# Optimization experiments

Measured on AMD Instinct MI355X. Metric: run time of the kernel, lower is better.

The kernel has to match this reference:

```python
import jax, jax.numpy as jnp
import numpy as np

BATCH = 16384
NUM_Q = 100000
NUM_TAGS = 1024
DIFF_FEAT = 3
DIM = 64
HIDDEN = 128


def setup_inputs() -> dict:
    key = jax.random.key(0)
    ks = jax.random.split(key, 10)
    questions = jax.random.randint(ks[0], (BATCH,), 0, NUM_Q, dtype=jnp.int64 if jax.config.jax_enable_x64 else jnp.int32)
    question_skill_targets = jax.random.randint(ks[1], (BATCH, NUM_TAGS), 0, 2, dtype=jnp.int32)
    difficulty_feats = jax.random.normal(ks[2], (BATCH, DIFF_FEAT), dtype=jnp.float32)
    Q_emb = jax.random.normal(ks[3], (NUM_Q, DIM), dtype=jnp.float32) * 0.02
    S_emb = jax.random.normal(ks[4], (NUM_TAGS, DIM), dtype=jnp.float32) * 0.02
    W_diff = jax.random.normal(ks[5], (DIFF_FEAT, DIM), dtype=jnp.float32) * 0.1
    b_diff = jnp.zeros((DIM,), dtype=jnp.float32)
    W_fc = jax.random.normal(ks[6], (3 * DIM + 3, HIDDEN), dtype=jnp.float32) * 0.05
    b_fc = jnp.zeros((HIDDEN,), dtype=jnp.float32)
    W_out = jax.random.normal(ks[7], (HIDDEN, 1), dtype=jnp.float32) * 0.05
    b_out = jnp.zeros((1,), dtype=jnp.float32)
    return {"questions": questions, "question_skill_targets": question_skill_targets,
            "difficulty_feats": difficulty_feats, "Q_emb": Q_emb, "S_emb": S_emb,
            "W_diff": W_diff, "b_diff": b_diff, "W_fc": W_fc, "b_fc": b_fc,
            "W_out": W_out, "b_out": b_out}


def reference(questions, question_skill_targets, difficulty_feats,
              Q_emb, S_emb, W_diff, b_diff, W_fc, b_fc, W_out, b_out):
    # Ragged segment-mean over skill sets: mean of skill embeddings whose
    # multi-hot entry is nonzero == (T @ S) / count per row.
    t = question_skill_targets.astype(jnp.float32)            # [B, T]
    counts = jnp.sum(t, axis=1, keepdims=True)                # [B, 1] (>=1 w.h.p.)
    mu_skill = (t @ S_emb) / counts                           # [B, D]
    q = Q_emb[questions]                                      # [B, D]
    a = difficulty_feats @ W_diff + b_diff                    # [B, D]
    # PNN product layer: pairwise inner products + concat linear signals
    p12 = jnp.sum(q * mu_skill, axis=-1, keepdims=True)
    p13 = jnp.sum(q * a, axis=-1, keepdims=True)
    p23 = jnp.sum(mu_skill * a, axis=-1, keepdims=True)
    z = jnp.concatenate([q, mu_skill, a, p12, p13, p23], axis=-1)  # [B, 3D+3]
    e = jax.nn.relu(z @ W_fc + b_fc)                          # [B, H]
    p = jax.nn.sigmoid(e @ W_out + b_out)[:, 0]               # [B]
    return (e, p)
```

## Files before the change

### kernel.cpp

```cpp
#include <hip/hip_runtime.h>
#include <hip/hip_bf16.h>

#define BATCH   16384
#define NTAGS   1024
#define DIM     64
#define HID     128

typedef __attribute__((ext_vector_type(8))) short bf16x8;
typedef __attribute__((ext_vector_type(4))) float f32x4;

__device__ __forceinline__ unsigned short f2bf(float v) {
    unsigned u = __builtin_bit_cast(unsigned, v);
    return (unsigned short)((u + 0x7FFFu + ((u >> 16) & 1u)) >> 16);
}

__global__ __launch_bounds__(256) void prep_pack(const float* __restrict__ S,
                                                 const float* __restrict__ Wfc,
                                                 unsigned short* __restrict__ Spack,
                                                 unsigned short* __restrict__ Wp)
{
    int tid = blockIdx.x * 256 + threadIdx.x;
    if (tid < 65536) {
        int j = tid & 7, l = (tid >> 3) & 63, nf = (tid >> 9) & 3, ks = tid >> 11;
        int k = ks * 32 + (l >> 4) * 8 + j;
        int d = nf * 16 + (l & 15);
        Spack[tid] = f2bf(S[k * 64 + d]);
    } else {
        int t2 = tid - 65536;
        int j = t2 & 7, l = (t2 >> 3) & 63, ct = (t2 >> 9) & 7, kt = t2 >> 12;
        int k = kt * 32 + (l >> 4) * 8 + j;
        int col = ct * 16 + (l & 15);
        Wp[t2] = f2bf(Wfc[k * 128 + col]);
    }
}

__global__ __launch_bounds__(256) void fused_kernel(
    const int* __restrict__ questions, const int* __restrict__ T,
    const float* __restrict__ dfeat, const float* __restrict__ Qemb,
    const float* __restrict__ Wdiff, const float* __restrict__ bdiff,
    const float* __restrict__ Wfc, const float* __restrict__ bfc,
    const float* __restrict__ Wout, const float* __restrict__ bout,
    const unsigned short* __restrict__ Spack, const unsigned short* __restrict__ Wp,
    float* __restrict__ out_e, float* __restrict__ out_p)
{
    __shared__ alignas(16) float accred[4][16][68];
    __shared__ float cntred[4][16];
    __shared__ alignas(16) unsigned short zb[16][200];
    __shared__ float scal[16][3];
    __shared__ float pacc[16][4];

    const int tid  = threadIdx.x;
    const int lane = tid & 63;
    const int wid  = tid >> 6;
    const int g    = lane >> 4;
    const int rl   = lane & 15;
    const int rb   = blockIdx.x * 16;

    f32x4 a0{}, a1{}, a2{}, a3{}, ac{};
    bf16x8 ones;
#pragma unroll
    for (int j = 0; j < 8; ++j) ones[j] = (short)0x3F80;

    const int* tp = T + (rb + rl) * 1024 + wid * 256 + g * 8;
    const unsigned short* sp = Spack + (size_t)wid * 8 * 2048 + lane * 8;

#pragma unroll
    for (int ks = 0; ks < 8; ++ks) {
        int4 t0 = *(const int4*)(tp + ks * 32);
        int4 t1 = *(const int4*)(tp + ks * 32 + 4);
        bf16x8 af;
        af[0] = t0.x ? (short)0x3F80 : (short)0;
        af[1] = t0.y ? (short)0x3F80 : (short)0;
        af[2] = t0.z ? (short)0x3F80 : (short)0;
        af[3] = t0.w ? (short)0x3F80 : (short)0;
        af[4] = t1.x ? (short)0x3F80 : (short)0;
        af[5] = t1.y ? (short)0x3F80 : (short)0;
        af[6] = t1.z ? (short)0x3F80 : (short)0;
        af[7] = t1.w ? (short)0x3F80 : (short)0;

        const unsigned short* s2 = sp + ks * 2048;
        bf16x8 b0 = *(const bf16x8*)(s2);
        bf16x8 b1 = *(const bf16x8*)(s2 + 512);
        bf16x8 b2 = *(const bf16x8*)(s2 + 1024);
        bf16x8 b3 = *(const bf16x8*)(s2 + 1536);

        a0 = __builtin_amdgcn_mfma_f32_16x16x32_bf16(af, b0, a0, 0, 0, 0);
        a1 = __builtin_amdgcn_mfma_f32_16x16x32_bf16(af, b1, a1, 0, 0, 0);
        a2 = __builtin_amdgcn_mfma_f32_16x16x32_bf16(af, b2, a2, 0, 0, 0);
        a3 = __builtin_amdgcn_mfma_f32_16x16x32_bf16(af, b3, a3, 0, 0, 0);
        ac = __builtin_amdgcn_mfma_f32_16x16x32_bf16(af, ones, ac, 0, 0, 0);
    }

#pragma unroll
    for (int r = 0; r < 4; ++r) {
        int row = g * 4 + r;
        accred[wid][row][rl]      = a0[r];
        accred[wid][row][16 + rl] = a1[r];
        accred[wid][row][32 + rl] = a2[r];
        accred[wid][row][48 + rl] = a3[r];
    }
    if (rl == 0) {
#pragma unroll
        for (int r = 0; r < 4; ++r) cntred[wid][g * 4 + r] = ac[r];
    }
    __syncthreads();

    {
        int r = tid >> 4, c16 = tid & 15, d0 = c16 * 4;
        float c = cntred[0][r] + cntred[1][r] + cntred[2][r] + cntred[3][r];
        float inv = 1.f / c;
        float4 m0 = *(const float4*)&accred[0][r][d0];
        float4 m1 = *(const float4*)&accred[1][r][d0];
        float4 m2 = *(const float4*)&accred[2][r][d0];
        float4 m3 = *(const float4*)&accred[3][r][d0];
        float mu[4];
        mu[0] = (m0.x + m1.x + m2.x + m3.x) * inv;
        mu[1] = (m0.y + m1.y + m2.y + m3.y) * inv;
        mu[2] = (m0.z + m1.z + m2.z + m3.z) * inv;
        mu[3] = (m0.w + m1.w + m2.w + m3.w) * inv;

        int qi = questions[rb + r];
        float4 q4 = *(const float4*)(Qemb + (size_t)qi * 64 + d0);
        float q[4] = {q4.x, q4.y, q4.z, q4.w};

        float f0 = dfeat[(rb + r) * 3 + 0];
        float f1 = dfeat[(rb + r) * 3 + 1];
        float f2 = dfeat[(rb + r) * 3 + 2];
        float aa[4];
#pragma unroll
        for (int d = 0; d < 4; ++d)
            aa[d] = bdiff[d0 + d] + f0 * Wdiff[d0 + d] + f1 * Wdiff[64 + d0 + d]
                  + f2 * Wdiff[128 + d0 + d];

        ushort4 qv, mv, av;
        qv.x = f2bf(q[0]);  qv.y = f2bf(q[1]);  qv.z = f2bf(q[2]);  qv.w = f2bf(q[3]);
        mv.x = f2bf(mu[0]); mv.y = f2bf(mu[1]); mv.z = f2bf(mu[2]); mv.w = f2bf(mu[3]);
        av.x = f2bf(aa[0]); av.y = f2bf(aa[1]); av.z = f2bf(aa[2]); av.w = f2bf(aa[3]);
        *(ushort4*)&zb[r][d0]       = qv;
        *(ushort4*)&zb[r][64 + d0]  = mv;
        *(ushort4*)&zb[r][128 + d0] = av;

        float s12 = 0.f, s13 = 0.f, s23 = 0.f;
#pragma unroll
        for (int d = 0; d < 4; ++d) {
            s12 += q[d] * mu[d];
            s13 += q[d] * aa[d];
            s23 += mu[d] * aa[d];
        }
#pragma unroll
        for (int off = 1; off < 16; off <<= 1) {
            s12 += __shfl_xor(s12, off);
            s13 += __shfl_xor(s13, off);
            s23 += __shfl_xor(s23, off);
        }
        if (c16 == 0) { scal[r][0] = s12; scal[r][1] = s13; scal[r][2] = s23; }
    }
    __syncthreads();

    {
        bf16x8 afr[6];
#pragma unroll
        for (int kt = 0; kt < 6; ++kt)
            afr[kt] = *(const bf16x8*)&zb[rl][kt * 32 + g * 8];

        float pr0 = 0.f, pr1 = 0.f, pr2 = 0.f, pr3 = 0.f;
#pragma unroll
        for (int c2 = 0; c2 < 2; ++c2) {
            int ct = wid * 2 + c2;
            f32x4 e{};
            const unsigned short* wp = Wp + (size_t)ct * 512 + lane * 8;
#pragma unroll
            for (int kt = 0; kt < 6; ++kt) {
                bf16x8 bfr = *(const bf16x8*)(wp + (size_t)kt * 4096);
                e = __builtin_amdgcn_mfma_f32_16x16x32_bf16(afr[kt], bfr, e, 0, 0, 0);
            }
            int h = ct * 16 + rl;
            float w192 = Wfc[192 * 128 + h];
            float w193 = Wfc[193 * 128 + h];
            float w194 = Wfc[194 * 128 + h];
            float bb = bfc[h];
            float wo = Wout[h];
#pragma unroll
            for (int r = 0; r < 4; ++r) {
                int row = g * 4 + r;
                float ev = e[r] + bb + scal[row][0] * w192 + scal[row][1] * w193
                         + scal[row][2] * w194;
                ev = ev > 0.f ? ev : 0.f;
                out_e[(size_t)(rb + row) * 128 + h] = ev;
                float pc = ev * wo;
                if (r == 0) pr0 += pc; else if (r == 1) pr1 += pc;
                else if (r == 2) pr2 += pc; else pr3 += pc;
            }
        }
#pragma unroll
        for (int off = 1; off < 16; off <<= 1) {
            pr0 += __shfl_xor(pr0, off);
            pr1 += __shfl_xor(pr1, off);
            pr2 += __shfl_xor(pr2, off);
            pr3 += __shfl_xor(pr3, off);
        }
        if (rl == 0) {
            pacc[g * 4 + 0][wid] = pr0;
            pacc[g * 4 + 1][wid] = pr1;
            pacc[g * 4 + 2][wid] = pr2;
            pacc[g * 4 + 3][wid] = pr3;
        }
    }
    __syncthreads();
    if (tid < 16) {
        float v = pacc[tid][0] + pacc[tid][1] + pacc[tid][2] + pacc[tid][3] + bout[0];
        out_p[rb + tid] = 1.f / (1.f + expf(-v));
    }
}

extern "C" void kernel_launch(void* const* d_in, const int* in_sizes, int n_in,
                              void* d_out, int out_size, void* d_ws, size_t ws_size,
                              hipStream_t stream)
{
    const int*   questions = (const int*)d_in[0];
    const int*   T         = (const int*)d_in[1];
    const float* dfeat     = (const float*)d_in[2];
    const float* Qemb      = (const float*)d_in[3];
    const float* Semb      = (const float*)d_in[4];
    const float* Wdiff     = (const float*)d_in[5];
    const float* bdiff     = (const float*)d_in[6];
    const float* Wfc       = (const float*)d_in[7];
    const float* bfc       = (const float*)d_in[8];
    const float* Wout      = (const float*)d_in[9];
    const float* bout      = (const float*)d_in[10];

    char* ws = (char*)d_ws;
    unsigned short* Spack = (unsigned short*)ws;
    unsigned short* Wp    = (unsigned short*)(ws + 131072);

    float* out_e = (float*)d_out;
    float* out_p = out_e + (size_t)BATCH * HID;

    hipLaunchKernelGGL(prep_pack, dim3(352), dim3(256), 0, stream, Semb, Wfc, Spack, Wp);
    hipLaunchKernelGGL(fused_kernel, dim3(BATCH / 16), dim3(256), 0, stream,
                       questions, T, dfeat, Qemb, Wdiff, bdiff, Wfc, bfc, Wout, bout,
                       Spack, Wp, out_e, out_p);
}
```

Baseline: 28.40 us.

## Pack multi-hot targets into LDS bitmask and derive counts via popcount

Each wave now loads the int32 multi-hot rows with contiguous per-lane reads, compresses them to one bit per tag in shared memory, then rebuilds bf16 A-fragments from the bits for the MFMA segment-sum. The row count comes from popcount plus a shuffle reduction instead of an extra MFMA against a ones vector. The aim is to make the 64 MB target read fully coalesced and to drop the fifth MFMA per step. In exchange it adds a barrier and some bit-manipulation ALU work before the matrix loop.

```diff
diff --git a/kernel.cpp b/kernel.cpp
--- a/kernel.cpp
+++ b/kernel.cpp
@@ -8,6 +8,7 @@
 
 typedef __attribute__((ext_vector_type(8))) short bf16x8;
 typedef __attribute__((ext_vector_type(4))) float f32x4;
+typedef __attribute__((ext_vector_type(4))) unsigned int u32x4;
 
 __device__ __forceinline__ unsigned short f2bf(float v) {
     unsigned u = __builtin_bit_cast(unsigned, v);
@@ -44,7 +45,7 @@
     float* __restrict__ out_e, float* __restrict__ out_p)
 {
     __shared__ alignas(16) float accred[4][16][68];
-    __shared__ float cntred[4][16];
+    __shared__ alignas(16) unsigned char bitsb[16][144];
     __shared__ alignas(16) unsigned short zb[16][200];
     __shared__ float scal[16][3];
     __shared__ float pacc[16][4];
@@ -56,39 +57,57 @@
     const int rl   = lane & 15;
     const int rb   = blockIdx.x * 16;
 
-    f32x4 a0{}, a1{}, a2{}, a3{}, ac{};
-    bf16x8 ones;
-#pragma unroll
-    for (int j = 0; j < 8; ++j) ones[j] = (short)0x3F80;
-
-    const int* tp = T + (rb + rl) * 1024 + wid * 256 + g * 8;
-    const unsigned short* sp = Spack + (size_t)wid * 8 * 2048 + lane * 8;
-
-#pragma unroll
-    for (int ks = 0; ks < 8; ++ks) {
-        int4 t0 = *(const int4*)(tp + ks * 32);
-        int4 t1 = *(const int4*)(tp + ks * 32 + 4);
-        bf16x8 af;
-        af[0] = t0.x ? (short)0x3F80 : (short)0;
-        af[1] = t0.y ? (short)0x3F80 : (short)0;
-        af[2] = t0.z ? (short)0x3F80 : (short)0;
-        af[3] = t0.w ? (short)0x3F80 : (short)0;
-        af[4] = t1.x ? (short)0x3F80 : (short)0;
-        af[5] = t1.y ? (short)0x3F80 : (short)0;
-        af[6] = t1.z ? (short)0x3F80 : (short)0;
-        af[7] = t1.w ? (short)0x3F80 : (short)0;
-
-        const unsigned short* s2 = sp + ks * 2048;
-        bf16x8 b0 = *(const bf16x8*)(s2);
-        bf16x8 b1 = *(const bf16x8*)(s2 + 512);
-        bf16x8 b2 = *(const bf16x8*)(s2 + 1024);
-        bf16x8 b3 = *(const bf16x8*)(s2 + 1536);
-
-        a0 = __builtin_amdgcn_mfma_f32_16x16x32_bf16(af, b0, a0, 0, 0, 0);
-        a1 = __builtin_amdgcn_mfma_f32_16x16x32_bf16(af, b1, a1, 0, 0, 0);
-        a2 = __builtin_amdgcn_mfma_f32_16x16x32_bf16(af, b2, a2, 0, 0, 0);
-        a3 = __builtin_amdgcn_mfma_f32_16x16x32_bf16(af, b3, a3, 0, 0, 0);
-        ac = __builtin_amdgcn_mfma_f32_16x16x32_bf16(af, ones, ac, 0, 0, 0);
+    {
+        const int* tp = T + (size_t)(rb + wid * 4) * 1024;
+#pragma unroll
+        for (int it = 0; it < 8; ++it) {
+            int idx = it * 64 + lane;
+            const int* p = tp + idx * 8;
+            int4 t0 = *(const int4*)(p);
+            int4 t1 = *(const int4*)(p + 4);
+            unsigned b = (unsigned)t0.x | ((unsigned)t0.y << 1) | ((unsigned)t0.z << 2)
+                       | ((unsigned)t0.w << 3) | ((unsigned)t1.x << 4) | ((unsigned)t1.y << 5)
+                       | ((unsigned)t1.z << 6) | ((unsigned)t1.w << 7);
+            int row  = wid * 4 + (idx >> 7);
+            int byt  = idx & 127;
+            bitsb[row][byt] = (unsigned char)b;
+        }
+    }
+    __syncthreads();
+
+    f32x4 a0{}, a1{}, a2{}, a3{};
+    {
+        const unsigned char* bp = &bitsb[rl][wid * 32];
+        u32x4 w0 = *(const u32x4*)(bp);
+        u32x4 w1 = *(const u32x4*)(bp + 16);
+        unsigned bw[8] = {w0[0], w0[1], w0[2], w0[3], w1[0], w1[1], w1[2], w1[3]};
+
+        const unsigned short* sp = Spack + (size_t)wid * 8 * 2048 + lane * 8;
+
+#pragma unroll
+        for (int ks = 0; ks < 8; ++ks) {
+            unsigned byte = (bw[ks] >> (g * 8)) & 0xFFu;
+            unsigned dw[4];
+#pragma unroll
+            for (int p = 0; p < 4; ++p) {
+                unsigned lo = (byte >> (2 * p)) & 1u;
+                unsigned hi = (byte >> (2 * p + 1)) & 1u;
+                dw[p] = lo * 0x3F80u | ((hi * 0x7Fu) << 23);
+            }
+            u32x4 dv = {dw[0], dw[1], dw[2], dw[3]};
+            bf16x8 af = __builtin_bit_cast(bf16x8, dv);
+
+            const unsigned short* s2 = sp + ks * 2048;
+            bf16x8 b0 = *(const bf16x8*)(s2);
+            bf16x8 b1 = *(const bf16x8*)(s2 + 512);
+            bf16x8 b2 = *(const bf16x8*)(s2 + 1024);
+            bf16x8 b3 = *(const bf16x8*)(s2 + 1536);
+
+            a0 = __builtin_amdgcn_mfma_f32_16x16x32_bf16(af, b0, a0, 0, 0, 0);
+            a1 = __builtin_amdgcn_mfma_f32_16x16x32_bf16(af, b1, a1, 0, 0, 0);
+            a2 = __builtin_amdgcn_mfma_f32_16x16x32_bf16(af, b2, a2, 0, 0, 0);
+            a3 = __builtin_amdgcn_mfma_f32_16x16x32_bf16(af, b3, a3, 0, 0, 0);
+        }
     }
 
 #pragma unroll
@@ -99,16 +118,17 @@
         accred[wid][row][32 + rl] = a2[r];
         accred[wid][row][48 + rl] = a3[r];
     }
-    if (rl == 0) {
-#pragma unroll
-        for (int r = 0; r < 4; ++r) cntred[wid][g * 4 + r] = ac[r];
-    }
     __syncthreads();
 
     {
         int r = tid >> 4, c16 = tid & 15, d0 = c16 * 4;
-        float c = cntred[0][r] + cntred[1][r] + cntred[2][r] + cntred[3][r];
-        float inv = 1.f / c;
+
+        const unsigned* bd = (const unsigned*)&bitsb[r][0];
+        int cb = __popc(bd[2 * c16]) + __popc(bd[2 * c16 + 1]);
+#pragma unroll
+        for (int off = 1; off < 16; off <<= 1) cb += __shfl_xor(cb, off);
+        float inv = 1.f / (float)cb;
+
         float4 m0 = *(const float4*)&accred[0][r][d0];
         float4 m1 = *(const float4*)&accred[1][r][d0];
         float4 m2 = *(const float4*)&accred[2][r][d0];
```

New measurement: 28.62 us. No clear change (+0.7%).

## Split skill GEMM into separate 32x32 MFMA kernel with bf16 partial sums

Applied to the files above, without the earlier changes.

Splits the fused kernel in two. A standalone GEMM kernel uses 32x32x16 MFMA tiles with a split-K of 4 and writes bf16 partial sums and integer counts to workspace. A tail kernel then reduces the partials and runs the product and FC layers. Counts now come from a scalar add instead of an extra ones-MFMA, and the prep packing is rewritten with coalesced reads. This adds an extra launch, an 8 MB partial-sum round trip through memory, and bf16 rounding of the partial sums.

```diff
diff --git a/kernel.cpp b/kernel.cpp
--- a/kernel.cpp
+++ b/kernel.cpp
@@ -6,45 +6,103 @@
 #define DIM     64
 #define HID     128
 
-typedef __attribute__((ext_vector_type(8))) short bf16x8;
-typedef __attribute__((ext_vector_type(4))) float f32x4;
+typedef __attribute__((ext_vector_type(8)))  short bf16x8;
+typedef __attribute__((ext_vector_type(4)))  float f32x4;
+typedef __attribute__((ext_vector_type(16))) float f32x16;
 
 __device__ __forceinline__ unsigned short f2bf(float v) {
     unsigned u = __builtin_bit_cast(unsigned, v);
     return (unsigned short)((u + 0x7FFFu + ((u >> 16) & 1u)) >> 16);
 }
-
-__global__ __launch_bounds__(256) void prep_pack(const float* __restrict__ S,
-                                                 const float* __restrict__ Wfc,
-                                                 unsigned short* __restrict__ Spack,
-                                                 unsigned short* __restrict__ Wp)
+__device__ __forceinline__ float bf2f(unsigned short u) {
+    return __builtin_bit_cast(float, ((unsigned)u) << 16);
+}
+
+__global__ __launch_bounds__(256) void prep_pack32(const float* __restrict__ S,
+                                                   const float* __restrict__ Wfc,
+                                                   unsigned short* __restrict__ Sp32,
+                                                   unsigned short* __restrict__ Wp)
 {
     int tid = blockIdx.x * 256 + threadIdx.x;
     if (tid < 65536) {
-        int j = tid & 7, l = (tid >> 3) & 63, nf = (tid >> 9) & 3, ks = tid >> 11;
-        int k = ks * 32 + (l >> 4) * 8 + j;
-        int d = nf * 16 + (l & 15);
-        Spack[tid] = f2bf(S[k * 64 + d]);
-    } else {
+        int k = tid >> 6, d = tid & 63;
+        float v = S[tid];
+        int ks = k >> 4, j = k & 7, kh = (k >> 3) & 1;
+        int nf = d >> 5, lane = (d & 31) + 32 * kh;
+        Sp32[((size_t)(ks * 2 + nf) * 64 + lane) * 8 + j] = f2bf(v);
+    } else if (tid < 65536 + 24576) {
         int t2 = tid - 65536;
-        int j = t2 & 7, l = (t2 >> 3) & 63, ct = (t2 >> 9) & 7, kt = t2 >> 12;
-        int k = kt * 32 + (l >> 4) * 8 + j;
-        int col = ct * 16 + (l & 15);
-        Wp[t2] = f2bf(Wfc[k * 128 + col]);
-    }
-}
-
-__global__ __launch_bounds__(256) void fused_kernel(
-    const int* __restrict__ questions, const int* __restrict__ T,
-    const float* __restrict__ dfeat, const float* __restrict__ Qemb,
+        int k = t2 >> 7, col = t2 & 127;
+        float v = Wfc[t2];
+        int kt = k >> 5, j = k & 7, l = ((k >> 3) & 3) * 16 + (col & 15), ct = col >> 4;
+        Wp[((size_t)(kt * 8 + ct) * 64 + l) * 8 + j] = f2bf(v);
+    }
+}
+
+__global__ __launch_bounds__(256) void gemm32(const int* __restrict__ T,
+                                              const unsigned short* __restrict__ Sp32,
+                                              unsigned short* __restrict__ musum_p,
+                                              float* __restrict__ cntp)
+{
+    const int lane = threadIdx.x & 63;
+    const int wid  = threadIdx.x >> 6;
+    const int gw   = blockIdx.x * 4 + wid;
+    const int mt   = gw >> 2;
+    const int ksp  = gw & 3;
+    const int r32  = lane & 31;
+    const int kh   = lane >> 5;
+
+    const int* tp = T + (size_t)(mt * 32 + r32) * 1024 + ksp * 256 + kh * 8;
+    const unsigned short* spb = Sp32 + (size_t)(ksp * 16) * 1024 + lane * 8;
+
+    f32x16 acc0{}, acc1{};
+    int c = 0;
+#pragma unroll
+    for (int st = 0; st < 16; ++st) {
+        int4 t0 = *(const int4*)(tp + st * 16);
+        int4 t1 = *(const int4*)(tp + st * 16 + 4);
+        c += t0.x + t0.y + t0.z + t0.w + t1.x + t1.y + t1.z + t1.w;
+        bf16x8 af;
+        af[0] = (short)((-t0.x) & 0x3F80);
+        af[1] = (short)((-t0.y) & 0x3F80);
+        af[2] = (short)((-t0.z) & 0x3F80);
+        af[3] = (short)((-t0.w) & 0x3F80);
+        af[4] = (short)((-t1.x) & 0x3F80);
+        af[5] = (short)((-t1.y) & 0x3F80);
+        af[6] = (short)((-t1.z) & 0x3F80);
+        af[7] = (short)((-t1.w) & 0x3F80);
+
+        const unsigned short* s2 = spb + st * 1024;
+        bf16x8 b0 = *(const bf16x8*)(s2);
+        bf16x8 b1 = *(const bf16x8*)(s2 + 512);
+
+        acc0 = __builtin_amdgcn_mfma_f32_32x32x16_bf16(af, b0, acc0, 0, 0, 0);
+        acc1 = __builtin_amdgcn_mfma_f32_32x32x16_bf16(af, b1, acc1, 0, 0, 0);
+    }
+
+    c += __shfl_xor(c, 32);
+    if (lane < 32) cntp[(size_t)(mt * 32 + lane) * 4 + ksp] = (float)c;
+
+    unsigned short* mo = musum_p + (size_t)ksp * BATCH * 64;
+#pragma unroll
+    for (int reg = 0; reg < 16; ++reg) {
+        int rr = (reg & 3) + 8 * (reg >> 2) + 4 * kh;
+        size_t base = (size_t)(mt * 32 + rr) * 64 + r32;
+        mo[base]      = f2bf(acc0[reg]);
+        mo[base + 32] = f2bf(acc1[reg]);
+    }
+}
+
+__global__ __launch_bounds__(256) void tail_kernel(
+    const int* __restrict__ questions, const float* __restrict__ dfeat,
+    const float* __restrict__ Qemb,
     const float* __restrict__ Wdiff, const float* __restrict__ bdiff,
     const float* __restrict__ Wfc, const float* __restrict__ bfc,
     const float* __restrict__ Wout, const float* __restrict__ bout,
-    const unsigned short* __restrict__ Spack, const unsigned short* __restrict__ Wp,
+    const unsigned short* __restrict__ musum_p, const float* __restrict__ cntp,
+    const unsigned short* __restrict__ Wp,
     float* __restrict__ out_e, float* __restrict__ out_p)
 {
-    __shared__ alignas(16) float accred[4][16][68];
-    __shared__ float cntred[4][16];
     __shared__ alignas(16) unsigned short zb[16][200];
     __shared__ float scal[16][3];
     __shared__ float pacc[16][4];
@@ -56,76 +114,28 @@
     const int rl   = lane & 15;
     const int rb   = blockIdx.x * 16;
 
-    f32x4 a0{}, a1{}, a2{}, a3{}, ac{};
-    bf16x8 ones;
-#pragma unroll
-    for (int j = 0; j < 8; ++j) ones[j] = (short)0x3F80;
-
-    const int* tp = T + (rb + rl) * 1024 + wid * 256 + g * 8;
-    const unsigned short* sp = Spack + (size_t)wid * 8 * 2048 + lane * 8;
-
-#pragma unroll
-    for (int ks = 0; ks < 8; ++ks) {
-        int4 t0 = *(const int4*)(tp + ks * 32);
-        int4 t1 = *(const int4*)(tp + ks * 32 + 4);
-        bf16x8 af;
-        af[0] = t0.x ? (short)0x3F80 : (short)0;
-        af[1] = t0.y ? (short)0x3F80 : (short)0;
-        af[2] = t0.z ? (short)0x3F80 : (short)0;
-        af[3] = t0.w ? (short)0x3F80 : (short)0;
-        af[4] = t1.x ? (short)0x3F80 : (short)0;
-        af[5] = t1.y ? (short)0x3F80 : (short)0;
-        af[6] = t1.z ? (short)0x3F80 : (short)0;
-        af[7] = t1.w ? (short)0x3F80 : (short)0;
-
-        const unsigned short* s2 = sp + ks * 2048;
-        bf16x8 b0 = *(const bf16x8*)(s2);
-        bf16x8 b1 = *(const bf16x8*)(s2 + 512);
-        bf16x8 b2 = *(const bf16x8*)(s2 + 1024);
-        bf16x8 b3 = *(const bf16x8*)(s2 + 1536);
-
-        a0 = __builtin_amdgcn_mfma_f32_16x16x32_bf16(af, b0, a0, 0, 0, 0);
-        a1 = __builtin_amdgcn_mfma_f32_16x16x32_bf16(af, b1, a1, 0, 0, 0);
-        a2 = __builtin_amdgcn_mfma_f32_16x16x32_bf16(af, b2, a2, 0, 0, 0);
-        a3 = __builtin_amdgcn_mfma_f32_16x16x32_bf16(af, b3, a3, 0, 0, 0);
-        ac = __builtin_amdgcn_mfma_f32_16x16x32_bf16(af, ones, ac, 0, 0, 0);
-    }
-
-#pragma unroll
-    for (int r = 0; r < 4; ++r) {
-        int row = g * 4 + r;
-        accred[wid][row][rl]      = a0[r];
-        accred[wid][row][16 + rl] = a1[r];
-        accred[wid][row][32 + rl] = a2[r];
-        accred[wid][row][48 + rl] = a3[r];
-    }
-    if (rl == 0) {
-#pragma unroll
-        for (int r = 0; r < 4; ++r) cntred[wid][g * 4 + r] = ac[r];
-    }
-    __syncthreads();
-
     {
         int r = tid >> 4, c16 = tid & 15, d0 = c16 * 4;
-        float c = cntred[0][r] + cntred[1][r] + cntred[2][r] + cntred[3][r];
-        float inv = 1.f / c;
-        float4 m0 = *(const float4*)&accred[0][r][d0];
-        float4 m1 = *(const float4*)&accred[1][r][d0];
-        float4 m2 = *(const float4*)&accred[2][r][d0];
-        float4 m3 = *(const float4*)&accred[3][r][d0];
-        float mu[4];
-        mu[0] = (m0.x + m1.x + m2.x + m3.x) * inv;
-        mu[1] = (m0.y + m1.y + m2.y + m3.y) * inv;
-        mu[2] = (m0.z + m1.z + m2.z + m3.z) * inv;
-        mu[3] = (m0.w + m1.w + m2.w + m3.w) * inv;
-
-        int qi = questions[rb + r];
+        int row = rb + r;
+
+        float4 cp = *(const float4*)&cntp[(size_t)row * 4];
+        float inv = 1.f / (cp.x + cp.y + cp.z + cp.w);
+
+        float m0 = 0.f, m1 = 0.f, m2 = 0.f, m3 = 0.f;
+#pragma unroll
+        for (int p = 0; p < 4; ++p) {
+            ushort4 mv = *(const ushort4*)&musum_p[((size_t)p * BATCH + row) * 64 + d0];
+            m0 += bf2f(mv.x); m1 += bf2f(mv.y); m2 += bf2f(mv.z); m3 += bf2f(mv.w);
+        }
+        float mu[4] = {m0 * inv, m1 * inv, m2 * inv, m3 * inv};
+
+        int qi = questions[row];
         float4 q4 = *(const float4*)(Qemb + (size_t)qi * 64 + d0);
         float q[4] = {q4.x, q4.y, q4.z, q4.w};
 
-        float f0 = dfeat[(rb + r) * 3 + 0];
-        float f1 = dfeat[(rb + r) * 3 + 1];
-        float f2 = dfeat[(rb + r) * 3 + 2];
+        float f0 = dfeat[row * 3 + 0];
+        float f1 = dfeat[row * 3 + 1];
+        float f2 = dfeat[row * 3 + 2];
         float aa[4];
 #pragma unroll
         for (int d = 0; d < 4; ++d)
@@ -230,14 +240,17 @@
     const float* bout      = (const float*)d_in[10];
 
     char* ws = (char*)d_ws;
-    unsigned short* Spack = (unsigned short*)ws;
-    unsigned short* Wp    = (unsigned short*)(ws + 131072);
+    unsigned short* Sp32    = (unsigned short*)ws;
+    unsigned short* Wp      = (unsigned short*)(ws + 131072);
+    unsigned short* musum_p = (unsigned short*)(ws + 262144);
+    float*          cntp    = (float*)(ws + 262144 + 8388608);
 
     float* out_e = (float*)d_out;
     float* out_p = out_e + (size_t)BATCH * HID;
 
-    hipLaunchKernelGGL(prep_pack, dim3(352), dim3(256), 0, stream, Semb, Wfc, Spack, Wp);
-    hipLaunchKernelGGL(fused_kernel, dim3(BATCH / 16), dim3(256), 0, stream,
-                       questions, T, dfeat, Qemb, Wdiff, bdiff, Wfc, bfc, Wout, bout,
-                       Spack, Wp, out_e, out_p);
-}
+    hipLaunchKernelGGL(prep_pack32, dim3(352), dim3(256), 0, stream, Semb, Wfc, Sp32, Wp);
+    hipLaunchKernelGGL(gemm32, dim3(512), dim3(256), 0, stream, T, Sp32, musum_p, cntp);
+    hipLaunchKernelGGL(tail_kernel, dim3(BATCH / 16), dim3(256), 0, stream,
+                       questions, dfeat, Qemb, Wdiff, bdiff, Wfc, bfc, Wout, bout,
+                       musum_p, cntp, Wp, out_e, out_p);
+}
```

Measured after the change: 31.67 us. 11.5% more time.

## Give each wavefront its own 16 rows, removing cross-wave reductions and barriers

Applied to the files above, without the earlier changes.

Work is reassigned so each wavefront owns 16 batch rows and runs the full 1024-tag reduction, the feature build and all 8 hidden column tiles itself. The block now covers 64 rows and has no __syncthreads. Skill counts come from an integer sum of the int inputs instead of a ones-MFMA, and the T loads are software-prefetched one step ahead. This removes LDS round-trips and block barriers, but gives each wave a much longer serial chain with only 16 rows per wave, which may leave memory latency less hidden. mu is now re-read from LDS as bf16 for the dot products, so it carries bf16 rounding, and the LDS handoffs within a wave rely on no explicit sync.

```diff
diff --git a/kernel.cpp b/kernel.cpp
--- a/kernel.cpp
+++ b/kernel.cpp
@@ -12,6 +12,9 @@
 __device__ __forceinline__ unsigned short f2bf(float v) {
     unsigned u = __builtin_bit_cast(unsigned, v);
     return (unsigned short)((u + 0x7FFFu + ((u >> 16) & 1u)) >> 16);
+}
+__device__ __forceinline__ float bf2f(unsigned short u) {
+    return __builtin_bit_cast(float, ((unsigned)u) << 16);
 }
 
 __global__ __launch_bounds__(256) void prep_pack(const float* __restrict__ S,
@@ -25,7 +28,7 @@
         int k = ks * 32 + (l >> 4) * 8 + j;
         int d = nf * 16 + (l & 15);
         Spack[tid] = f2bf(S[k * 64 + d]);
-    } else {
+    } else if (tid < 65536 + 24576) {
         int t2 = tid - 65536;
         int j = t2 & 7, l = (t2 >> 3) & 63, ct = (t2 >> 9) & 7, kt = t2 >> 12;
         int k = kt * 32 + (l >> 4) * 8 + j;
@@ -34,7 +37,7 @@
     }
 }
 
-__global__ __launch_bounds__(256) void fused_kernel(
+__global__ __launch_bounds__(256) void mega_kernel(
     const int* __restrict__ questions, const int* __restrict__ T,
     const float* __restrict__ dfeat, const float* __restrict__ Qemb,
     const float* __restrict__ Wdiff, const float* __restrict__ bdiff,
@@ -43,130 +46,152 @@
     const unsigned short* __restrict__ Spack, const unsigned short* __restrict__ Wp,
     float* __restrict__ out_e, float* __restrict__ out_p)
 {
-    __shared__ alignas(16) float accred[4][16][68];
-    __shared__ float cntred[4][16];
-    __shared__ alignas(16) unsigned short zb[16][200];
-    __shared__ float scal[16][3];
-    __shared__ float pacc[16][4];
+    __shared__ alignas(16) unsigned short zb[4][16][200];
+    __shared__ float cnt16[4][16];
+    __shared__ float scal[4][16][3];
 
     const int tid  = threadIdx.x;
     const int lane = tid & 63;
     const int wid  = tid >> 6;
     const int g    = lane >> 4;
     const int rl   = lane & 15;
-    const int rb   = blockIdx.x * 16;
-
-    f32x4 a0{}, a1{}, a2{}, a3{}, ac{};
-    bf16x8 ones;
-#pragma unroll
-    for (int j = 0; j < 8; ++j) ones[j] = (short)0x3F80;
-
-    const int* tp = T + (rb + rl) * 1024 + wid * 256 + g * 8;
-    const unsigned short* sp = Spack + (size_t)wid * 8 * 2048 + lane * 8;
-
-#pragma unroll
-    for (int ks = 0; ks < 8; ++ks) {
-        int4 t0 = *(const int4*)(tp + ks * 32);
-        int4 t1 = *(const int4*)(tp + ks * 32 + 4);
-        bf16x8 af;
-        af[0] = t0.x ? (short)0x3F80 : (short)0;
-        af[1] = t0.y ? (short)0x3F80 : (short)0;
-        af[2] = t0.z ? (short)0x3F80 : (short)0;
-        af[3] = t0.w ? (short)0x3F80 : (short)0;
-        af[4] = t1.x ? (short)0x3F80 : (short)0;
-        af[5] = t1.y ? (short)0x3F80 : (short)0;
-        af[6] = t1.z ? (short)0x3F80 : (short)0;
-        af[7] = t1.w ? (short)0x3F80 : (short)0;
-
-        const unsigned short* s2 = sp + ks * 2048;
-        bf16x8 b0 = *(const bf16x8*)(s2);
-        bf16x8 b1 = *(const bf16x8*)(s2 + 512);
-        bf16x8 b2 = *(const bf16x8*)(s2 + 1024);
-        bf16x8 b3 = *(const bf16x8*)(s2 + 1536);
-
-        a0 = __builtin_amdgcn_mfma_f32_16x16x32_bf16(af, b0, a0, 0, 0, 0);
-        a1 = __builtin_amdgcn_mfma_f32_16x16x32_bf16(af, b1, a1, 0, 0, 0);
-        a2 = __builtin_amdgcn_mfma_f32_16x16x32_bf16(af, b2, a2, 0, 0, 0);
-        a3 = __builtin_amdgcn_mfma_f32_16x16x32_bf16(af, b3, a3, 0, 0, 0);
-        ac = __builtin_amdgcn_mfma_f32_16x16x32_bf16(af, ones, ac, 0, 0, 0);
-    }
-
-#pragma unroll
-    for (int r = 0; r < 4; ++r) {
-        int row = g * 4 + r;
-        accred[wid][row][rl]      = a0[r];
-        accred[wid][row][16 + rl] = a1[r];
-        accred[wid][row][32 + rl] = a2[r];
-        accred[wid][row][48 + rl] = a3[r];
-    }
-    if (rl == 0) {
-#pragma unroll
-        for (int r = 0; r < 4; ++r) cntred[wid][g * 4 + r] = ac[r];
-    }
-    __syncthreads();
-
-    {
-        int r = tid >> 4, c16 = tid & 15, d0 = c16 * 4;
-        float c = cntred[0][r] + cntred[1][r] + cntred[2][r] + cntred[3][r];
-        float inv = 1.f / c;
-        float4 m0 = *(const float4*)&accred[0][r][d0];
-        float4 m1 = *(const float4*)&accred[1][r][d0];
-        float4 m2 = *(const float4*)&accred[2][r][d0];
-        float4 m3 = *(const float4*)&accred[3][r][d0];
-        float mu[4];
-        mu[0] = (m0.x + m1.x + m2.x + m3.x) * inv;
-        mu[1] = (m0.y + m1.y + m2.y + m3.y) * inv;
-        mu[2] = (m0.z + m1.z + m2.z + m3.z) * inv;
-        mu[3] = (m0.w + m1.w + m2.w + m3.w) * inv;
-
-        int qi = questions[rb + r];
-        float4 q4 = *(const float4*)(Qemb + (size_t)qi * 64 + d0);
-        float q[4] = {q4.x, q4.y, q4.z, q4.w};
-
-        float f0 = dfeat[(rb + r) * 3 + 0];
-        float f1 = dfeat[(rb + r) * 3 + 1];
-        float f2 = dfeat[(rb + r) * 3 + 2];
-        float aa[4];
-#pragma unroll
-        for (int d = 0; d < 4; ++d)
-            aa[d] = bdiff[d0 + d] + f0 * Wdiff[d0 + d] + f1 * Wdiff[64 + d0 + d]
-                  + f2 * Wdiff[128 + d0 + d];
-
-        ushort4 qv, mv, av;
-        qv.x = f2bf(q[0]);  qv.y = f2bf(q[1]);  qv.z = f2bf(q[2]);  qv.w = f2bf(q[3]);
-        mv.x = f2bf(mu[0]); mv.y = f2bf(mu[1]); mv.z = f2bf(mu[2]); mv.w = f2bf(mu[3]);
-        av.x = f2bf(aa[0]); av.y = f2bf(aa[1]); av.z = f2bf(aa[2]); av.w = f2bf(aa[3]);
-        *(ushort4*)&zb[r][d0]       = qv;
-        *(ushort4*)&zb[r][64 + d0]  = mv;
-        *(ushort4*)&zb[r][128 + d0] = av;
-
+    const int wrow = (blockIdx.x * 4 + wid) * 16;
+
+    unsigned short (*z)[200] = zb[wid];
+    float* cw = cnt16[wid];
+    float (*sc)[3] = scal[wid];
+
+    f32x4 a0{}, a1{}, a2{}, a3{};
+    int c = 0;
+    {
+        const int* tp = T + (size_t)(wrow + rl) * 1024 + g * 8;
+        const unsigned short* sp = Spack + lane * 8;
+
+        int4 t0 = *(const int4*)(tp);
+        int4 t1 = *(const int4*)(tp + 4);
+#pragma unroll
+        for (int st = 0; st < 32; ++st) {
+            int4 c0 = t0, c1 = t1;
+            if (st < 31) {
+                t0 = *(const int4*)(tp + (st + 1) * 32);
+                t1 = *(const int4*)(tp + (st + 1) * 32 + 4);
+            }
+            c += c0.x + c0.y + c0.z + c0.w + c1.x + c1.y + c1.z + c1.w;
+            bf16x8 af;
+            af[0] = (short)((-c0.x) & 0x3F80);
+            af[1] = (short)((-c0.y) & 0x3F80);
+            af[2] = (short)((-c0.z) & 0x3F80);
+            af[3] = (short)((-c0.w) & 0x3F80);
+            af[4] = (short)((-c1.x) & 0x3F80);
+            af[5] = (short)((-c1.y) & 0x3F80);
+            af[6] = (short)((-c1.z) & 0x3F80);
+            af[7] = (short)((-c1.w) & 0x3F80);
+
+            const unsigned short* s2 = sp + st * 2048;
+            bf16x8 b0 = *(const bf16x8*)(s2);
+            bf16x8 b1 = *(const bf16x8*)(s2 + 512);
+            bf16x8 b2 = *(const bf16x8*)(s2 + 1024);
+            bf16x8 b3 = *(const bf16x8*)(s2 + 1536);
+
+            a0 = __builtin_amdgcn_mfma_f32_16x16x32_bf16(af, b0, a0, 0, 0, 0);
+            a1 = __builtin_amdgcn_mfma_f32_16x16x32_bf16(af, b1, a1, 0, 0, 0);
+            a2 = __builtin_amdgcn_mfma_f32_16x16x32_bf16(af, b2, a2, 0, 0, 0);
+            a3 = __builtin_amdgcn_mfma_f32_16x16x32_bf16(af, b3, a3, 0, 0, 0);
+        }
+    }
+    c += __shfl_xor(c, 16);
+    c += __shfl_xor(c, 32);
+    if (lane < 16) cw[lane] = (float)c;
+
+    {
+        float inv[4];
+#pragma unroll
+        for (int r = 0; r < 4; ++r) inv[r] = 1.f / cw[g * 4 + r];
+#pragma unroll
+        for (int r = 0; r < 4; ++r) {
+            int row = g * 4 + r;
+            z[row][64 + rl]      = f2bf(a0[r] * inv[r]);
+            z[row][64 + 16 + rl] = f2bf(a1[r] * inv[r]);
+            z[row][64 + 32 + rl] = f2bf(a2[r] * inv[r]);
+            z[row][64 + 48 + rl] = f2bf(a3[r] * inv[r]);
+        }
+    }
+
+    {
+        int r = lane >> 2, q4 = lane & 3, d0 = q4 * 16;
+        int row = wrow + r;
+        int qi = questions[row];
+
+        float q[16], aa[16], mu[16];
+#pragma unroll
+        for (int b = 0; b < 4; ++b) {
+            float4 v = *(const float4*)(Qemb + (size_t)qi * 64 + d0 + b * 4);
+            q[b * 4 + 0] = v.x; q[b * 4 + 1] = v.y; q[b * 4 + 2] = v.z; q[b * 4 + 3] = v.w;
+        }
+        float f0 = dfeat[row * 3 + 0];
+        float f1 = dfeat[row * 3 + 1];
+        float f2 = dfeat[row * 3 + 2];
+#pragma unroll
+        for (int b = 0; b < 4; ++b) {
+            float4 w0 = *(const float4*)(Wdiff + d0 + b * 4);
+            float4 w1 = *(const float4*)(Wdiff + 64 + d0 + b * 4);
+            float4 w2 = *(const float4*)(Wdiff + 128 + d0 + b * 4);
+            float4 bd = *(const float4*)(bdiff + d0 + b * 4);
+            aa[b * 4 + 0] = bd.x + f0 * w0.x + f1 * w1.x + f2 * w2.x;
+            aa[b * 4 + 1] = bd.y + f0 * w0.y + f1 * w1.y + f2 * w2.y;
+            aa[b * 4 + 2] = bd.z + f0 * w0.z + f1 * w1.z + f2 * w2.z;
+            aa[b * 4 + 3] = bd.w + f0 * w0.w + f1 * w1.w + f2 * w2.w;
+        }
+#pragma unroll
+        for (int b = 0; b < 2; ++b) {
+            ushort4 m0 = *(const ushort4*)&z[r][64 + d0 + b * 8];
+            ushort4 m1 = *(const ushort4*)&z[r][64 + d0 + b * 8 + 4];
+            mu[b * 8 + 0] = bf2f(m0.x); mu[b * 8 + 1] = bf2f(m0.y);
+            mu[b * 8 + 2] = bf2f(m0.z); mu[b * 8 + 3] = bf2f(m0.w);
+            mu[b * 8 + 4] = bf2f(m1.x); mu[b * 8 + 5] = bf2f(m1.y);
+            mu[b * 8 + 6] = bf2f(m1.z); mu[b * 8 + 7] = bf2f(m1.w);
+        }
         float s12 = 0.f, s13 = 0.f, s23 = 0.f;
 #pragma unroll
-        for (int d = 0; d < 4; ++d) {
+        for (int d = 0; d < 16; ++d) {
             s12 += q[d] * mu[d];
             s13 += q[d] * aa[d];
             s23 += mu[d] * aa[d];
         }
-#pragma unroll
-        for (int off = 1; off < 16; off <<= 1) {
-            s12 += __shfl_xor(s12, off);
-            s13 += __shfl_xor(s13, off);
-            s23 += __shfl_xor(s23, off);
-        }
-        if (c16 == 0) { scal[r][0] = s12; scal[r][1] = s13; scal[r][2] = s23; }
-    }
-    __syncthreads();
+        s12 += __shfl_xor(s12, 1); s12 += __shfl_xor(s12, 2);
+        s13 += __shfl_xor(s13, 1); s13 += __shfl_xor(s13, 2);
+        s23 += __shfl_xor(s23, 1); s23 += __shfl_xor(s23, 2);
+        if (q4 == 0) { sc[r][0] = s12; sc[r][1] = s13; sc[r][2] = s23; }
+
+        ushort4 v;
+#pragma unroll
+        for (int b = 0; b < 4; ++b) {
+            v.x = f2bf(q[b * 4 + 0]); v.y = f2bf(q[b * 4 + 1]);
+            v.z = f2bf(q[b * 4 + 2]); v.w = f2bf(q[b * 4 + 3]);
+            *(ushort4*)&z[r][d0 + b * 4] = v;
+        }
+#pragma unroll
+        for (int b = 0; b < 4; ++b) {
+            v.x = f2bf(aa[b * 4 + 0]); v.y = f2bf(aa[b * 4 + 1]);
+            v.z = f2bf(aa[b * 4 + 2]); v.w = f2bf(aa[b * 4 + 3]);
+            *(ushort4*)&z[r][128 + d0 + b * 4] = v;
+        }
+    }
 
     {
         bf16x8 afr[6];
 #pragma unroll
         for (int kt = 0; kt < 6; ++kt)
-            afr[kt] = *(const bf16x8*)&zb[rl][kt * 32 + g * 8];
+            afr[kt] = *(const bf16x8*)&z[rl][kt * 32 + g * 8];
+
+        float s0 = sc[g * 4 + 0][0], s1 = sc[g * 4 + 0][1], s2 = sc[g * 4 + 0][2];
+        float t0_ = sc[g * 4 + 1][0], t1_ = sc[g * 4 + 1][1], t2_ = sc[g * 4 + 1][2];
+        float u0 = sc[g * 4 + 2][0], u1 = sc[g * 4 + 2][1], u2 = sc[g * 4 + 2][2];
+        float v0 = sc[g * 4 + 3][0], v1 = sc[g * 4 + 3][1], v2 = sc[g * 4 + 3][2];
 
         float pr0 = 0.f, pr1 = 0.f, pr2 = 0.f, pr3 = 0.f;
 #pragma unroll
-        for (int c2 = 0; c2 < 2; ++c2) {
-            int ct = wid * 2 + c2;
+        for (int ct = 0; ct < 8; ++ct) {
             f32x4 e{};
             const unsigned short* wp = Wp + (size_t)ct * 512 + lane * 8;
 #pragma unroll
@@ -180,17 +205,20 @@
             float w194 = Wfc[194 * 128 + h];
             float bb = bfc[h];
             float wo = Wout[h];
-#pragma unroll
-            for (int r = 0; r < 4; ++r) {
-                int row = g * 4 + r;
-                float ev = e[r] + bb + scal[row][0] * w192 + scal[row][1] * w193
-                         + scal[row][2] * w194;
-                ev = ev > 0.f ? ev : 0.f;
-                out_e[(size_t)(rb + row) * 128 + h] = ev;
-                float pc = ev * wo;
-                if (r == 0) pr0 += pc; else if (r == 1) pr1 += pc;
-                else if (r == 2) pr2 += pc; else pr3 += pc;
-            }
+
+            float ev;
+            ev = e[0] + bb + s0 * w192 + s1 * w193 + s2 * w194;
+            ev = ev > 0.f ? ev : 0.f;
+            out_e[(size_t)(wrow + g * 4 + 0) * 128 + h] = ev;  pr0 += ev * wo;
+            ev = e[1] + bb + t0_ * w192 + t1_ * w193 + t2_ * w194;
+            ev = ev > 0.f ? ev : 0.f;
+            out_e[(size_t)(wrow + g * 4 + 1) * 128 + h] = ev;  pr1 += ev * wo;
+            ev = e[2] + bb + u0 * w192 + u1 * w193 + u2 * w194;
+            ev = ev > 0.f ? ev : 0.f;
+            out_e[(size_t)(wrow + g * 4 + 2) * 128 + h] = ev;  pr2 += ev * wo;
+            ev = e[3] + bb + v0 * w192 + v1 * w193 + v2 * w194;
+            ev = ev > 0.f ? ev : 0.f;
+            out_e[(size_t)(wrow + g * 4 + 3) * 128 + h] = ev;  pr3 += ev * wo;
         }
 #pragma unroll
         for (int off = 1; off < 16; off <<= 1) {
@@ -200,16 +228,12 @@
             pr3 += __shfl_xor(pr3, off);
         }
         if (rl == 0) {
-            pacc[g * 4 + 0][wid] = pr0;
-            pacc[g * 4 + 1][wid] = pr1;
-            pacc[g * 4 + 2][wid] = pr2;
-            pacc[g * 4 + 3][wid] = pr3;
-        }
-    }
-    __syncthreads();
-    if (tid < 16) {
-        float v = pacc[tid][0] + pacc[tid][1] + pacc[tid][2] + pacc[tid][3] + bout[0];
-        out_p[rb + tid] = 1.f / (1.f + expf(-v));
+            float bo = bout[0];
+            out_p[wrow + g * 4 + 0] = 1.f / (1.f + expf(-(pr0 + bo)));
+            out_p[wrow + g * 4 + 1] = 1.f / (1.f + expf(-(pr1 + bo)));
+            out_p[wrow + g * 4 + 2] = 1.f / (1.f + expf(-(pr2 + bo)));
+            out_p[wrow + g * 4 + 3] = 1.f / (1.f + expf(-(pr3 + bo)));
+        }
     }
 }
 
@@ -237,7 +261,7 @@
     float* out_p = out_e + (size_t)BATCH * HID;
 
     hipLaunchKernelGGL(prep_pack, dim3(352), dim3(256), 0, stream, Semb, Wfc, Spack, Wp);
-    hipLaunchKernelGGL(fused_kernel, dim3(BATCH / 16), dim3(256), 0, stream,
+    hipLaunchKernelGGL(mega_kernel, dim3(BATCH / 64), dim3(256), 0, stream,
                        questions, T, dfeat, Qemb, Wdiff, bdiff, Wfc, bfc, Wout, bout,
                        Spack, Wp, out_e, out_p);
 }
```

After: 29.12 us. 1.03x slower.
